# Kernel optimization log

Measured on AMD Instinct MI355X. Metric: run time of the kernel, lower is better.

## Reference

```python
import jax, jax.numpy as jnp
import numpy as np

EMBED_DIM = 1024
NUM_HEADS = 16
HEAD_DIM = EMBED_DIM // NUM_HEADS
N_PATCHES = 220
ROPE_BASE = 10000.0
EPS = 1e-6


def rms_norm(x, g):
    # x: [..., d]
    rms = jnp.sqrt(jnp.mean(x * x, axis=-1, keepdims=True) + EPS)
    return g * (x / rms)


def apply_rope(x):
    # torchtune-style interleaved RoPE. x: [b, s, h, d]
    b, s, h, d = x.shape
    theta = 1.0 / (ROPE_BASE ** (jnp.arange(0, d, 2, dtype=jnp.float32) / d))  # [d/2]
    ang = jnp.arange(s, dtype=jnp.float32)[:, None] * theta[None, :]           # [s, d/2]
    cos = jnp.cos(ang)[None, :, None, :]
    sin = jnp.sin(ang)[None, :, None, :]
    xs = x.reshape(b, s, h, d // 2, 2)
    x0, x1 = xs[..., 0], xs[..., 1]
    out = jnp.stack([x0 * cos - x1 * sin, x1 * cos + x0 * sin], axis=-1)
    return out.reshape(b, s, h, d).astype(x.dtype)


def attention_block(x, w_qkv, w_proj, b_proj, q_gain, k_gain):
    # x: [N, S, C]; one SDPA branch (shared by spatial & temporal paths)
    N, S, C = x.shape
    H, D = NUM_HEADS, HEAD_DIM
    qkv = jnp.einsum('nsc,ec->nse', x, w_qkv).reshape(N, S, 3, H, D)
    q, k, v = qkv[:, :, 0], qkv[:, :, 1], qkv[:, :, 2]  # [N, S, H, D]
    q = apply_rope(rms_norm(q, q_gain))
    k = apply_rope(rms_norm(k, k_gain))
    scale = 1.0 / jnp.sqrt(jnp.float32(D))
    scores = jnp.einsum('nqhd,nkhd->nhqk', q, k) * scale
    attn = jax.nn.softmax(scores, axis=-1)
    out = jnp.einsum('nhqk,nkhd->nqhd', attn, v).reshape(N, S, C)
    return jnp.einsum('nsc,ec->nse', out, w_proj) + b_proj


def setup_inputs() -> dict:
    key = jax.random.key(0)
    ks = jax.random.split(key, 8)
    E = EMBED_DIM
    sd = 1.0 / np.sqrt(E)
    x = jax.random.normal(ks[0], (4, 5280, E), dtype=jnp.float32)
    w_sqkv = jax.random.uniform(ks[1], (3 * E, E), jnp.float32, -sd, sd)
    w_sproj = jax.random.uniform(ks[2], (E, E), jnp.float32, -sd, sd)
    b_sproj = jax.random.uniform(ks[3], (E,), jnp.float32, -sd, sd)
    w_tqkv = jax.random.uniform(ks[4], (3 * E, E), jnp.float32, -sd, sd)
    w_tproj = jax.random.uniform(ks[5], (E, E), jnp.float32, -sd, sd)
    b_tproj = jax.random.uniform(ks[6], (E,), jnp.float32, -sd, sd)
    g = jnp.ones((HEAD_DIM,), jnp.float32)
    return {
        'x': x,
        'w_sqkv': w_sqkv, 'w_sproj': w_sproj, 'b_sproj': b_sproj,
        'w_tqkv': w_tqkv, 'w_tproj': w_tproj, 'b_tproj': b_tproj,
        'sq_gain': g, 'sk_gain': g, 'tq_gain': g, 'tk_gain': g,
    }


def reference(x, w_sqkv, w_sproj, b_sproj, w_tqkv, w_tproj, b_tproj,
              sq_gain, sk_gain, tq_gain, tk_gain):
    B, T, C = x.shape
    P = N_PATCHES
    F = T // P
    # spatial attention per frame: (b f) p c
    xs = x.reshape(B, F, P, C).reshape(B * F, P, C)
    out_s = attention_block(xs, w_sqkv, w_sproj, b_sproj, sq_gain, sk_gain)
    # temporal attention per patch: (b p) f c
    xt = out_s.reshape(B, F, P, C).transpose(0, 2, 1, 3).reshape(B * P, F, C)
    out_t = attention_block(xt, w_tqkv, w_tproj, b_tproj, tq_gain, tk_gain)
    # (b p) f c -> b (f p) c
    out = out_t.reshape(B, P, F, C).transpose(0, 2, 1, 3).reshape(B, F * P, C)
    return out
```

## Files before the change

kernel.cpp:

```cpp
#include <hip/hip_runtime.h>

typedef _Float16 f16;
typedef _Float16 f16x8 __attribute__((ext_vector_type(8)));
typedef f16x8 f16x8a __attribute__((may_alias));
typedef float f32x4 __attribute__((ext_vector_type(4)));

#define NTOK 21120
#define SCALE_Q 0.18033688f

__device__ __forceinline__ void gll16(const void* g, void* l) {
  __builtin_amdgcn_global_load_lds(
      (const __attribute__((address_space(1))) unsigned int*)g,
      (__attribute__((address_space(3))) unsigned int*)l, 16, 0, 0);
}

__device__ __forceinline__ unsigned int pack2(float a, float b) {
  union { f16 h[2]; unsigned int u; } c;
  c.h[0] = (f16)a; c.h[1] = (f16)b;
  return c.u;
}
__device__ __forceinline__ unsigned short f2h(float a) {
  union { f16 h; unsigned short u; } c; c.h = (f16)a; return c.u;
}

__global__ __launch_bounds__(256) void cast_kernel(
    const float* __restrict__ in, unsigned short* __restrict__ out, int n4) {
  int i = blockIdx.x * 256 + threadIdx.x;
  if (i >= n4) return;
  float4 v = ((const float4*)in)[i];
  uint2 o;
  o.x = pack2(v.x, v.y);
  o.y = pack2(v.z, v.w);
  ((uint2*)out)[i] = o;
}

__global__ __launch_bounds__(256) void transpose_cast_kernel(
    const float* __restrict__ in, unsigned short* __restrict__ out) {
  __shared__ float tile[32][33];
  int bx = blockIdx.x & 31, by = blockIdx.x >> 5;
  int tx = threadIdx.x & 31, ty = threadIdx.x >> 5;
#pragma unroll
  for (int i = 0; i < 32; i += 8)
    tile[ty + i][tx] = in[(size_t)(by * 32 + ty + i) * 1024 + bx * 32 + tx];
  __syncthreads();
#pragma unroll
  for (int i = 0; i < 32; i += 8)
    out[(size_t)(bx * 32 + ty + i) * 1024 + by * 32 + tx] = f2h(tile[tx][ty + i]);
}

__global__ __launch_bounds__(256) void bias_combine_kernel(
    const float* __restrict__ w, const float* __restrict__ b, float* __restrict__ bc) {
  int e = blockIdx.x * 256 + threadIdx.x;
  if (e >= 3072) return;
  const float4* wr = (const float4*)(w + (size_t)e * 1024);
  const float4* b4 = (const float4*)b;
  float s = 0.f;
  for (int c = 0; c < 256; ++c) {
    float4 wv = wr[c], bv = b4[c];
    s += wv.x * bv.x + wv.y * bv.y + wv.z * bv.z + wv.w * bv.w;
  }
  bc[e] = s;
}

__global__ __launch_bounds__(256) void rope_table_kernel(float2* tabS, float2* tabT) {
  int t = blockIdx.x * 256 + threadIdx.x;
  const float lb = logf(10000.0f) * (1.0f / 32.0f);
  if (t < 220 * 32) {
    int s = t >> 5, i = t & 31;
    float theta = expf(-(float)i * lb);
    float ang = (float)s * theta;
    tabS[t] = make_float2(cosf(ang), sinf(ang));
  } else if (t < 220 * 32 + 24 * 32) {
    int u = t - 220 * 32;
    int s = u >> 5, i = u & 31;
    float theta = expf(-(float)i * lb);
    float ang = (float)s * theta;
    tabT[u] = make_float2(cosf(ang), sinf(ang));
  }
}

__global__ __launch_bounds__(256) void gemm_bt(
    const unsigned short* __restrict__ A, const unsigned short* __restrict__ B,
    const float* __restrict__ bias, void* __restrict__ C,
    int M, int N, int K, int outmode,
    const float2* __restrict__ tab, const float* __restrict__ gq,
    const float* __restrict__ gk, int mode) {
  __shared__ __align__(16) unsigned short sh[16384];
  unsigned short* As = sh;
  unsigned short* Bs = sh + 8192;
  const int tid = threadIdx.x;
  const int w = tid >> 6, lane = tid & 63;
  const int l15 = lane & 15, quad = lane >> 4;
  const int wr = w >> 1, wc = w & 1;

  const int ntn = N >> 7;
  const int stride = ntn << 3;
  const int g = blockIdx.x / stride, r = blockIdx.x % stride;
  const int tn = r % ntn, tm = g * 8 + r / ntn;

  f32x4 acc[4][4];
#pragma unroll
  for (int a = 0; a < 4; ++a)
#pragma unroll
    for (int b = 0; b < 4; ++b) acc[a][b] = (f32x4){0.f, 0.f, 0.f, 0.f};

  const int srow = tid >> 3;
  const int schk = tid & 7;
  const size_t arow0 = (size_t)tm * 128;
  const size_t brow0 = (size_t)tn * 128;
  const int nk = K >> 6;

  for (int kt = 0; kt < nk; ++kt) {
    __syncthreads();
    const int kb = kt << 6;
#pragma unroll
    for (int rd = 0; rd < 4; ++rd) {
      int row = rd * 32 + srow;
      int sc = (schk ^ (row & 7)) * 8;
      gll16(A + (arow0 + row) * K + kb + sc, (char*)As + rd * 4096 + tid * 16);
      gll16(B + (brow0 + row) * K + kb + sc, (char*)Bs + rd * 4096 + tid * 16);
    }
    __syncthreads();
#pragma unroll
    for (int kk = 0; kk < 2; ++kk) {
      f16x8 af[4], bf[4];
#pragma unroll
      for (int mt = 0; mt < 4; ++mt) {
        int ra = wr * 64 + mt * 16 + l15;
        af[mt] = *(const f16x8a*)((const char*)As + ra * 128 + (((kk * 4 + quad) ^ (ra & 7)) * 16));
        int rb = wc * 64 + mt * 16 + l15;
        bf[mt] = *(const f16x8a*)((const char*)Bs + rb * 128 + (((kk * 4 + quad) ^ (rb & 7)) * 16));
      }
#pragma unroll
      for (int mt = 0; mt < 4; ++mt)
#pragma unroll
        for (int nt = 0; nt < 4; ++nt)
          acc[mt][nt] = __builtin_amdgcn_mfma_f32_16x16x32_f16(af[mt], bf[nt], acc[mt][nt], 0, 0, 0);
    }
  }

  float bv[4];
#pragma unroll
  for (int nt = 0; nt < 4; ++nt) bv[nt] = 0.f;
  if (bias != nullptr && outmode != 3) {
#pragma unroll
    for (int nt = 0; nt < 4; ++nt) bv[nt] = bias[tn * 128 + wc * 64 + nt * 16 + l15];
  }

  if (outmode == 2) {
    float* shf = (float*)sh;
#pragma unroll
    for (int mt = 0; mt < 4; ++mt) {
      __syncthreads();
#pragma unroll
      for (int nt = 0; nt < 4; ++nt)
#pragma unroll
        for (int rg = 0; rg < 4; ++rg)
          shf[(wr * 16 + quad * 4 + rg) * 132 + wc * 64 + nt * 16 + l15] = acc[mt][nt][rg] + bv[nt];
      __syncthreads();
      int l = tid >> 3, c8 = tid & 7;
      int grow = tm * 128 + ((l >> 4) << 6) + mt * 16 + (l & 15);
      float4* dst = (float4*)((float*)C + (size_t)grow * N + tn * 128 + c8 * 16);
      const float4* srcp = (const float4*)(shf + l * 132 + c8 * 16);
#pragma unroll
      for (int c = 0; c < 4; ++c) dst[c] = srcp[c];
    }
    return;
  }

  if (outmode == 3 && tn < 16) {
    const int qtile = tn < 8;
    const float* gg = qtile ? gq : gk;
    float* shf = (float*)sh;
    const int sub = tid & 3, pr = tid >> 2;
    const int l = pr >> 1, head = pr & 1;
    float bl[16];
    if (bias != nullptr) {
      const float4* bsrc = (const float4*)(bias + tn * 128 + head * 64 + sub * 16);
#pragma unroll
      for (int c = 0; c < 4; ++c) {
        float4 bb = bsrc[c];
        bl[c * 4 + 0] = bb.x; bl[c * 4 + 1] = bb.y; bl[c * 4 + 2] = bb.z; bl[c * 4 + 3] = bb.w;
      }
    } else {
#pragma unroll
      for (int j = 0; j < 16; ++j) bl[j] = 0.f;
    }
#pragma unroll
    for (int mt = 0; mt < 4; ++mt) {
      __syncthreads();
#pragma unroll
      for (int nt = 0; nt < 4; ++nt)
#pragma unroll
        for (int rg = 0; rg < 4; ++rg)
          shf[(wr * 16 + quad * 4 + rg) * 132 + wc * 64 + nt * 16 + l15] = acc[mt][nt][rg];
      __syncthreads();
      int grow = tm * 128 + ((l >> 4) << 6) + mt * 16 + (l & 15);
      int pos = (mode == 0) ? (grow % 220) : ((grow / 220) % 24);
      float v[16];
      const float4* vsrc = (const float4*)(shf + l * 132 + head * 64 + sub * 16);
#pragma unroll
      for (int c = 0; c < 4; ++c) {
        float4 t4 = vsrc[c];
        v[c * 4 + 0] = t4.x + bl[c * 4 + 0];
        v[c * 4 + 1] = t4.y + bl[c * 4 + 1];
        v[c * 4 + 2] = t4.z + bl[c * 4 + 2];
        v[c * 4 + 3] = t4.w + bl[c * 4 + 3];
      }
      float ssq = 0.f;
#pragma unroll
      for (int j = 0; j < 16; ++j) ssq += v[j] * v[j];
      ssq += __shfl_xor(ssq, 1);
      ssq += __shfl_xor(ssq, 2);
      float rr = rsqrtf(ssq * (1.0f / 64.0f) + 1e-6f);
      if (qtile) rr *= SCALE_Q;
      const float2* cs = tab + pos * 32 + sub * 8;
      const float2* g2 = (const float2*)gg + sub * 8;
      unsigned int o8[8];
#pragma unroll
      for (int jj = 0; jj < 8; ++jj) {
        float2 c = cs[jj], gp = g2[jj];
        float a = v[2 * jj] * rr * gp.x, b = v[2 * jj + 1] * rr * gp.y;
        o8[jj] = pack2(a * c.x - b * c.y, b * c.x + a * c.y);
      }
      unsigned short* dstp = (unsigned short*)C + (size_t)grow * N + tn * 128 + head * 64 + sub * 16;
      ((uint4*)dstp)[0] = ((const uint4*)o8)[0];
      ((uint4*)dstp)[1] = ((const uint4*)o8)[1];
    }
    return;
  }

  if (outmode == 3 && bias != nullptr) {
#pragma unroll
    for (int nt = 0; nt < 4; ++nt) bv[nt] = bias[tn * 128 + wc * 64 + nt * 16 + l15];
  }

  unsigned short* Cs = (unsigned short*)C;
#pragma unroll
  for (int p = 0; p < 2; ++p) {
    __syncthreads();
#pragma unroll
    for (int mi = 0; mi < 2; ++mi) {
      int mt = p * 2 + mi;
      int rl = wr * 32 + mi * 16 + quad * 4;
#pragma unroll
      for (int nt = 0; nt < 4; ++nt) {
        int cl = wc * 64 + nt * 16 + l15;
#pragma unroll
        for (int rg = 0; rg < 4; ++rg)
          sh[(rl + rg) * 136 + cl] = f2h(acc[mt][nt][rg] + bv[nt]);
      }
    }
    __syncthreads();
#pragma unroll
    for (int c = 0; c < 4; ++c) {
      int rl = c * 16 + (tid >> 4), cx = tid & 15;
      int grow = tm * 128 + ((rl >> 5) << 6) + p * 32 + (rl & 31);
      uint4 v = *(const uint4*)&sh[rl * 136 + cx * 8];
      *(uint4*)&Cs[(size_t)grow * N + tn * 128 + cx * 8] = v;
    }
  }
}

__global__ __launch_bounds__(256) void attn_spatial(
    const unsigned short* __restrict__ qkv, unsigned short* __restrict__ aout) {
  __shared__ __align__(16) unsigned short sh[30720];
  unsigned short* Kls = sh;
  unsigned short* Vt = sh + 8192;
  unsigned short* P = sh + 22528;
  const int tid = threadIdx.x;
  const int w = tid >> 6, lane = tid & 63;
  const int l15 = lane & 15, quad = lane >> 4;
  const int n = blockIdx.x >> 4, h = blockIdx.x & 15;
  const size_t tb = (size_t)n * 220;
  const unsigned short* qbase = qkv + tb * 3072 + h * 64;

  f16x8 aq[4][2];
#pragma unroll
  for (int mt = 0; mt < 4; ++mt) {
    int row = w * 64 + mt * 16 + l15;
    if (row > 219) row = 219;
#pragma unroll
    for (int c = 0; c < 2; ++c)
      aq[mt][c] = *(const f16x8a*)(qbase + (size_t)row * 3072 + c * 32 + quad * 8);
  }
  if (tid < 220) {
    const uint4* src = (const uint4*)(qbase + (size_t)tid * 3072 + 2048);
    uint4 vv[8];
#pragma unroll
    for (int c = 0; c < 8; ++c) vv[c] = src[c];
    const unsigned short* us = (const unsigned short*)vv;
#pragma unroll
    for (int d = 0; d < 64; ++d) Vt[d * 224 + tid] = us[d];
  } else if (tid < 224) {
#pragma unroll
    for (int d = 0; d < 64; ++d) Vt[d * 224 + tid] = 0;
  }

  float lsum[4][4];
  f32x4 o[4][4];
#pragma unroll
  for (int mt = 0; mt < 4; ++mt)
#pragma unroll
    for (int rg = 0; rg < 4; ++rg) lsum[mt][rg] = 0.f;
#pragma unroll
  for (int mt = 0; mt < 4; ++mt)
#pragma unroll
    for (int nt = 0; nt < 4; ++nt) o[mt][nt] = (f32x4){0.f, 0.f, 0.f, 0.f};

  const int xr = (l15 & 3) ^ ((l15 >> 2) & 3);
  unsigned short* Pw = P + w * 2048;

  for (int half = 0; half < 2; ++half) {
    const int k0 = half * 128;
    const int nslot = half ? 736 : 1024;
#pragma unroll
    for (int k = 0; k < 4; ++k) {
      int slot = k * 256 + tid;
      if (slot < nslot) {
        int rl = slot >> 3, c = slot & 7;
        gll16(qbase + (size_t)(k0 + rl) * 3072 + 1024 + ((c ^ (rl & 7)) * 8),
              (char*)Kls + k * 4096 + w * 1024);
      }
    }
    __syncthreads();
    const int nci = half ? 3 : 4;
    for (int ci = 0; ci < nci; ++ci) {
      const int cig = half * 4 + ci;
      f16x8 bk[2][2];
#pragma unroll
      for (int ct = 0; ct < 2; ++ct) {
        int rl = ci * 32 + ct * 16 + l15;
#pragma unroll
        for (int c = 0; c < 2; ++c)
          bk[ct][c] = *(const f16x8a*)((const char*)Kls + rl * 128 + (((quad + 4 * c) ^ (rl & 7)) * 16));
      }
      f32x4 sc[4][2];
#pragma unroll
      for (int mt = 0; mt < 4; ++mt)
#pragma unroll
        for (int ct = 0; ct < 2; ++ct) {
          f32x4 z = (f32x4){0.f, 0.f, 0.f, 0.f};
          z = __builtin_amdgcn_mfma_f32_16x16x32_f16(aq[mt][0], bk[ct][0], z, 0, 0, 0);
          sc[mt][ct] = __builtin_amdgcn_mfma_f32_16x16x32_f16(aq[mt][1], bk[ct][1], z, 0, 0, 0);
        }
      const int okk = (cig * 32 + 16 + l15) < 220;
#pragma unroll
      for (int mt = 0; mt < 4; ++mt)
#pragma unroll
        for (int rg = 0; rg < 4; ++rg) {
          float p0 = exp2f(sc[mt][0][rg]);
          float p1 = okk ? exp2f(sc[mt][1][rg]) : 0.0f;
          lsum[mt][rg] += p0 + p1;
          int xw = quad ^ rg;
          unsigned short* pb = Pw + (mt * 16 + quad * 4 + rg) * 32;
          pb[(((l15 >> 3) ^ xw) * 8) + (l15 & 7)] = f2h(p0);
          pb[(((2 + (l15 >> 3)) ^ xw) * 8) + (l15 & 7)] = f2h(p1);
        }
      __asm__ volatile("s_waitcnt lgkmcnt(0)" ::: "memory");
      f16x8 ap[4], bv[4];
#pragma unroll
      for (int mt = 0; mt < 4; ++mt)
        ap[mt] = *(const f16x8a*)((const char*)Pw + (mt * 16 + l15) * 64 + (quad ^ xr) * 16);
#pragma unroll
      for (int nt = 0; nt < 4; ++nt)
        bv[nt] = *(const f16x8a*)((const char*)Vt + (nt * 16 + l15) * 448 + cig * 64 + quad * 16);
#pragma unroll
      for (int mt = 0; mt < 4; ++mt)
#pragma unroll
        for (int nt = 0; nt < 4; ++nt)
          o[mt][nt] = __builtin_amdgcn_mfma_f32_16x16x32_f16(ap[mt], bv[nt], o[mt][nt], 0, 0, 0);
    }
    __syncthreads();
  }

#pragma unroll
  for (int mt = 0; mt < 4; ++mt)
#pragma unroll
    for (int rg = 0; rg < 4; ++rg) {
      float l = lsum[mt][rg];
      l += __shfl_xor(l, 1);
      l += __shfl_xor(l, 2);
      l += __shfl_xor(l, 4);
      l += __shfl_xor(l, 8);
      int s = w * 64 + mt * 16 + quad * 4 + rg;
      if (s < 220) {
        float inv = 1.0f / l;
        unsigned short* dst = aout + (tb + s) * 1024 + h * 64;
#pragma unroll
        for (int nt = 0; nt < 4; ++nt) dst[nt * 16 + l15] = f2h(o[mt][nt][rg] * inv);
      }
    }
}

__global__ __launch_bounds__(256) void attn_temporal(
    const unsigned short* __restrict__ qkv, unsigned short* __restrict__ aout) {
  __shared__ __align__(16) unsigned short sh[14336];
  const int tid = threadIdx.x;
  const int w = tid >> 6, lane = tid & 63;
  const int l15 = lane & 15, quad = lane >> 4;
  const int b = blockIdx.x / 880;
  const int rem = blockIdx.x % 880;
  const int p = rem >> 2, hq = rem & 3;
  const int h = hq * 4 + w;
  unsigned short* Vtw = sh + w * 2560;
  unsigned short* Pw = sh + 10240 + w * 1024;
  const unsigned short* base = qkv + ((size_t)(b * 24) * 220 + p) * 3072 + h * 64;
  const size_t fs = (size_t)220 * 3072;

  {
    int r = lane >> 1, hf = lane & 1;
    if (r < 24) {
      const uint4* src = (const uint4*)(base + r * fs + 2048 + hf * 32);
      uint4 vv[4];
#pragma unroll
      for (int c = 0; c < 4; ++c) vv[c] = src[c];
      const unsigned short* us = (const unsigned short*)vv;
#pragma unroll
      for (int j = 0; j < 32; ++j) Vtw[(hf * 32 + j) * 40 + r] = us[j];
    } else {
#pragma unroll
      for (int j = 0; j < 32; ++j) Vtw[(hf * 32 + j) * 40 + r] = 0;
    }
  }
  f16x8 aq[2][2], bk[2][2];
#pragma unroll
  for (int mt = 0; mt < 2; ++mt) {
    int row = mt * 16 + l15;
    if (row > 23) row = 23;
#pragma unroll
    for (int c = 0; c < 2; ++c)
      aq[mt][c] = *(const f16x8a*)(base + row * fs + c * 32 + quad * 8);
  }
#pragma unroll
  for (int ct = 0; ct < 2; ++ct) {
    int row = ct * 16 + l15;
    if (row > 23) row = 23;
#pragma unroll
    for (int c = 0; c < 2; ++c)
      bk[ct][c] = *(const f16x8a*)(base + row * fs + 1024 + c * 32 + quad * 8);
  }
  f32x4 sc[2][2];
#pragma unroll
  for (int mt = 0; mt < 2; ++mt)
#pragma unroll
    for (int ct = 0; ct < 2; ++ct) {
      f32x4 z = (f32x4){0.f, 0.f, 0.f, 0.f};
      z = __builtin_amdgcn_mfma_f32_16x16x32_f16(aq[mt][0], bk[ct][0], z, 0, 0, 0);
      sc[mt][ct] = __builtin_amdgcn_mfma_f32_16x16x32_f16(aq[mt][1], bk[ct][1], z, 0, 0, 0);
    }
  const int xr = (l15 & 3) ^ ((l15 >> 2) & 3);
  const int okk = l15 < 8;
  float lr[2][4];
#pragma unroll
  for (int mt = 0; mt < 2; ++mt)
#pragma unroll
    for (int rg = 0; rg < 4; ++rg) {
      float p0 = exp2f(sc[mt][0][rg]);
      float p1 = okk ? exp2f(sc[mt][1][rg]) : 0.0f;
      float rs = p0 + p1;
      rs += __shfl_xor(rs, 1);
      rs += __shfl_xor(rs, 2);
      rs += __shfl_xor(rs, 4);
      rs += __shfl_xor(rs, 8);
      lr[mt][rg] = rs;
      int xw = quad ^ rg;
      unsigned short* pb = Pw + (mt * 16 + quad * 4 + rg) * 32;
      pb[(((l15 >> 3) ^ xw) * 8) + (l15 & 7)] = f2h(p0);
      pb[(((2 + (l15 >> 3)) ^ xw) * 8) + (l15 & 7)] = f2h(p1);
    }
  __asm__ volatile("s_waitcnt lgkmcnt(0)" ::: "memory");
  f16x8 ap[2], bv[4];
#pragma unroll
  for (int mt = 0; mt < 2; ++mt)
    ap[mt] = *(const f16x8a*)((const char*)Pw + (mt * 16 + l15) * 64 + (quad ^ xr) * 16);
#pragma unroll
  for (int nt = 0; nt < 4; ++nt)
    bv[nt] = *(const f16x8a*)((const char*)Vtw + (nt * 16 + l15) * 80 + quad * 16);
  f32x4 o[2][4];
#pragma unroll
  for (int mt = 0; mt < 2; ++mt)
#pragma unroll
    for (int nt = 0; nt < 4; ++nt) {
      f32x4 z = (f32x4){0.f, 0.f, 0.f, 0.f};
      o[mt][nt] = __builtin_amdgcn_mfma_f32_16x16x32_f16(ap[mt], bv[nt], z, 0, 0, 0);
    }
#pragma unroll
  for (int mt = 0; mt < 2; ++mt)
#pragma unroll
    for (int rg = 0; rg < 4; ++rg) {
      int s = mt * 16 + quad * 4 + rg;
      if (s < 24) {
        float inv = 1.0f / lr[mt][rg];
        unsigned short* dst = aout + ((size_t)(b * 24 + s) * 220 + p) * 1024 + h * 64;
#pragma unroll
        for (int nt = 0; nt < 4; ++nt) dst[nt * 16 + l15] = f2h(o[mt][nt][rg] * inv);
      }
    }
}

extern "C" void kernel_launch(void* const* d_in, const int* in_sizes, int n_in,
                              void* d_out, int out_size, void* d_ws, size_t ws_size,
                              hipStream_t stream) {
  (void)in_sizes; (void)n_in; (void)out_size; (void)ws_size;
  const float* x = (const float*)d_in[0];
  const float* wsqkv = (const float*)d_in[1];
  const float* wsproj = (const float*)d_in[2];
  const float* bsproj = (const float*)d_in[3];
  const float* wtqkv = (const float*)d_in[4];
  const float* wtproj = (const float*)d_in[5];
  const float* btproj = (const float*)d_in[6];
  const float* sqg = (const float*)d_in[7];
  const float* skg = (const float*)d_in[8];
  const float* tqg = (const float*)d_in[9];
  const float* tkg = (const float*)d_in[10];

  char* ws = (char*)d_ws;
  size_t off = 0;
  auto alloc = [&](size_t bytes) {
    char* ptr = ws + off;
    off += (bytes + 255) & ~(size_t)255;
    return ptr;
  };
  unsigned short* xb = (unsigned short*)alloc((size_t)NTOK * 1024 * 2);
  unsigned short* qkvb = (unsigned short*)alloc((size_t)NTOK * 3072 * 2);
  unsigned short* aoutb = (unsigned short*)alloc((size_t)NTOK * 1024 * 2);
  unsigned short* wsqkvb = (unsigned short*)alloc((size_t)3072 * 1024 * 2);
  unsigned short* wsprojTb = (unsigned short*)alloc((size_t)1024 * 1024 * 2);
  unsigned short* wtqkvb = (unsigned short*)alloc((size_t)3072 * 1024 * 2);
  unsigned short* wtprojb = (unsigned short*)alloc((size_t)1024 * 1024 * 2);
  unsigned short* wcb = (unsigned short*)alloc((size_t)3072 * 1024 * 2);
  float* bcb = (float*)alloc(3072 * 4);
  float2* tabS = (float2*)alloc(220 * 32 * 8);
  float2* tabT = (float2*)alloc(24 * 32 * 8);

  dim3 blk(256);
  cast_kernel<<<21120, blk, 0, stream>>>(x, xb, 5406720);
  cast_kernel<<<3072, blk, 0, stream>>>(wsqkv, wsqkvb, 786432);
  cast_kernel<<<3072, blk, 0, stream>>>(wtqkv, wtqkvb, 786432);
  cast_kernel<<<1024, blk, 0, stream>>>(wtproj, wtprojb, 262144);
  transpose_cast_kernel<<<1024, blk, 0, stream>>>(wsproj, wsprojTb);
  bias_combine_kernel<<<12, blk, 0, stream>>>(wtqkv, bsproj, bcb);
  rope_table_kernel<<<31, blk, 0, stream>>>(tabS, tabT);

  gemm_bt<<<dim3(24 * 8), blk, 0, stream>>>(wtqkvb, wsprojTb, nullptr, wcb, 3072, 1024, 1024, 0,
                                            nullptr, nullptr, nullptr, 0);

  gemm_bt<<<dim3(165 * 24), blk, 0, stream>>>(xb, wsqkvb, nullptr, qkvb, NTOK, 3072, 1024, 3,
                                              tabS, sqg, skg, 0);
  attn_spatial<<<dim3(1536), blk, 0, stream>>>(qkvb, aoutb);
  gemm_bt<<<dim3(165 * 24), blk, 0, stream>>>(aoutb, wcb, bcb, qkvb, NTOK, 3072, 1024, 3,
                                              tabT, tqg, tkg, 1);
  attn_temporal<<<dim3(3520), blk, 0, stream>>>(qkvb, aoutb);
  gemm_bt<<<dim3(165 * 8), blk, 0, stream>>>(aoutb, wtprojb, btproj, (float*)d_out, NTOK, 1024, 1024, 2,
                                             nullptr, nullptr, nullptr, 0);
}
```

Measured before the change: 811.3 us.

## Replace 128-tile GEMMs with 256x256 pipelined 512-thread GEMM kernel

Adds a new GEMM kernel with 256x256 tiles, 8 waves, a four-slot LDS ring fed by global_load_lds and explicit vmcnt waits, s_setprio around MFMA bursts, and XCD-aware workgroup remapping. The fused RMSNorm+RoPE and fp32 epilogues are moved into the new kernel, using DPP cross-lane reductions. The activation buffers are padded to a multiple of 256 rows and the pad is zeroed so the last tile can read past the real rows without bounds checks. The goal is more data reuse per tile and better overlap of loads with MFMA. The cost is 128 KB of LDS per block, higher register pressure, and extra memset launches.

```diff
diff --git a/kernel.cpp b/kernel.cpp
--- a/kernel.cpp
+++ b/kernel.cpp
@@ -6,6 +6,7 @@
 typedef float f32x4 __attribute__((ext_vector_type(4)));
 
 #define NTOK 21120
+#define MPAD 21248
 #define SCALE_Q 0.18033688f
 
 __device__ __forceinline__ void gll16(const void* g, void* l) {
@@ -21,6 +22,14 @@
 }
 __device__ __forceinline__ unsigned short f2h(float a) {
   union { f16 h; unsigned short u; } c; c.h = (f16)a; return c.u;
+}
+
+template <int C>
+__device__ __forceinline__ float dppf(float x) {
+  union { float f; int i; } u, r;
+  u.f = x;
+  r.i = __builtin_amdgcn_update_dpp(0, u.i, C, 0xf, 0xf, true);
+  return r.f;
 }
 
 __global__ __launch_bounds__(256) void cast_kernel(
@@ -139,102 +148,6 @@
     }
   }
 
-  float bv[4];
-#pragma unroll
-  for (int nt = 0; nt < 4; ++nt) bv[nt] = 0.f;
-  if (bias != nullptr && outmode != 3) {
-#pragma unroll
-    for (int nt = 0; nt < 4; ++nt) bv[nt] = bias[tn * 128 + wc * 64 + nt * 16 + l15];
-  }
-
-  if (outmode == 2) {
-    float* shf = (float*)sh;
-#pragma unroll
-    for (int mt = 0; mt < 4; ++mt) {
-      __syncthreads();
-#pragma unroll
-      for (int nt = 0; nt < 4; ++nt)
-#pragma unroll
-        for (int rg = 0; rg < 4; ++rg)
-          shf[(wr * 16 + quad * 4 + rg) * 132 + wc * 64 + nt * 16 + l15] = acc[mt][nt][rg] + bv[nt];
-      __syncthreads();
-      int l = tid >> 3, c8 = tid & 7;
-      int grow = tm * 128 + ((l >> 4) << 6) + mt * 16 + (l & 15);
-      float4* dst = (float4*)((float*)C + (size_t)grow * N + tn * 128 + c8 * 16);
-      const float4* srcp = (const float4*)(shf + l * 132 + c8 * 16);
-#pragma unroll
-      for (int c = 0; c < 4; ++c) dst[c] = srcp[c];
-    }
-    return;
-  }
-
-  if (outmode == 3 && tn < 16) {
-    const int qtile = tn < 8;
-    const float* gg = qtile ? gq : gk;
-    float* shf = (float*)sh;
-    const int sub = tid & 3, pr = tid >> 2;
-    const int l = pr >> 1, head = pr & 1;
-    float bl[16];
-    if (bias != nullptr) {
-      const float4* bsrc = (const float4*)(bias + tn * 128 + head * 64 + sub * 16);
-#pragma unroll
-      for (int c = 0; c < 4; ++c) {
-        float4 bb = bsrc[c];
-        bl[c * 4 + 0] = bb.x; bl[c * 4 + 1] = bb.y; bl[c * 4 + 2] = bb.z; bl[c * 4 + 3] = bb.w;
-      }
-    } else {
-#pragma unroll
-      for (int j = 0; j < 16; ++j) bl[j] = 0.f;
-    }
-#pragma unroll
-    for (int mt = 0; mt < 4; ++mt) {
-      __syncthreads();
-#pragma unroll
-      for (int nt = 0; nt < 4; ++nt)
-#pragma unroll
-        for (int rg = 0; rg < 4; ++rg)
-          shf[(wr * 16 + quad * 4 + rg) * 132 + wc * 64 + nt * 16 + l15] = acc[mt][nt][rg];
-      __syncthreads();
-      int grow = tm * 128 + ((l >> 4) << 6) + mt * 16 + (l & 15);
-      int pos = (mode == 0) ? (grow % 220) : ((grow / 220) % 24);
-      float v[16];
-      const float4* vsrc = (const float4*)(shf + l * 132 + head * 64 + sub * 16);
-#pragma unroll
-      for (int c = 0; c < 4; ++c) {
-        float4 t4 = vsrc[c];
-        v[c * 4 + 0] = t4.x + bl[c * 4 + 0];
-        v[c * 4 + 1] = t4.y + bl[c * 4 + 1];
-        v[c * 4 + 2] = t4.z + bl[c * 4 + 2];
-        v[c * 4 + 3] = t4.w + bl[c * 4 + 3];
-      }
-      float ssq = 0.f;
-#pragma unroll
-      for (int j = 0; j < 16; ++j) ssq += v[j] * v[j];
-      ssq += __shfl_xor(ssq, 1);
-      ssq += __shfl_xor(ssq, 2);
-      float rr = rsqrtf(ssq * (1.0f / 64.0f) + 1e-6f);
-      if (qtile) rr *= SCALE_Q;
-      const float2* cs = tab + pos * 32 + sub * 8;
-      const float2* g2 = (const float2*)gg + sub * 8;
-      unsigned int o8[8];
-#pragma unroll
-      for (int jj = 0; jj < 8; ++jj) {
-        float2 c = cs[jj], gp = g2[jj];
-        float a = v[2 * jj] * rr * gp.x, b = v[2 * jj + 1] * rr * gp.y;
-        o8[jj] = pack2(a * c.x - b * c.y, b * c.x + a * c.y);
-      }
-      unsigned short* dstp = (unsigned short*)C + (size_t)grow * N + tn * 128 + head * 64 + sub * 16;
-      ((uint4*)dstp)[0] = ((const uint4*)o8)[0];
-      ((uint4*)dstp)[1] = ((const uint4*)o8)[1];
-    }
-    return;
-  }
-
-  if (outmode == 3 && bias != nullptr) {
-#pragma unroll
-    for (int nt = 0; nt < 4; ++nt) bv[nt] = bias[tn * 128 + wc * 64 + nt * 16 + l15];
-  }
-
   unsigned short* Cs = (unsigned short*)C;
 #pragma unroll
   for (int p = 0; p < 2; ++p) {
@@ -248,7 +161,7 @@
         int cl = wc * 64 + nt * 16 + l15;
 #pragma unroll
         for (int rg = 0; rg < 4; ++rg)
-          sh[(rl + rg) * 136 + cl] = f2h(acc[mt][nt][rg] + bv[nt]);
+          sh[(rl + rg) * 136 + cl] = f2h(acc[mt][nt][rg]);
       }
     }
     __syncthreads();
@@ -258,6 +171,257 @@
       int grow = tm * 128 + ((rl >> 5) << 6) + p * 32 + (rl & 31);
       uint4 v = *(const uint4*)&sh[rl * 136 + cx * 8];
       *(uint4*)&Cs[(size_t)grow * N + tn * 128 + cx * 8] = v;
+    }
+  }
+}
+
+#define FENCE() asm volatile("" ::: "memory")
+#define BAR() do { FENCE(); __builtin_amdgcn_s_barrier(); FENCE(); } while (0)
+#define WAITV(N) asm volatile("s_waitcnt vmcnt(" #N ")" ::: "memory")
+#define LDA(sl, i) (*(const f16x8a*)(As + (sl) * 16384 + sA[i]))
+#define LDB(sl, i) (*(const f16x8a*)(Bs + (sl) * 16384 + sB[i]))
+#define STAGE_A(u, sl) do { \
+    gll16(aS0 + (size_t)(u) * 32, As + (sl) * 16384 + tid * 16); \
+    gll16(aS1 + (size_t)(u) * 32, As + (sl) * 16384 + 8192 + tid * 16); \
+  } while (0)
+#define STAGE_B(u, sl) do { \
+    gll16(bS0 + (size_t)(u) * 32, Bs + (sl) * 16384 + tid * 16); \
+    gll16(bS1 + (size_t)(u) * 32, Bs + (sl) * 16384 + 8192 + tid * 16); \
+  } while (0)
+#define MM16(QB, A0_, A1_, A2_, A3_, B0_, B1_, B2_, B3_) do { \
+    acc[QB + 0][0] = __builtin_amdgcn_mfma_f32_16x16x32_f16(A0_, B0_, acc[QB + 0][0], 0, 0, 0); \
+    acc[QB + 0][1] = __builtin_amdgcn_mfma_f32_16x16x32_f16(A0_, B1_, acc[QB + 0][1], 0, 0, 0); \
+    acc[QB + 0][2] = __builtin_amdgcn_mfma_f32_16x16x32_f16(A0_, B2_, acc[QB + 0][2], 0, 0, 0); \
+    acc[QB + 0][3] = __builtin_amdgcn_mfma_f32_16x16x32_f16(A0_, B3_, acc[QB + 0][3], 0, 0, 0); \
+    acc[QB + 1][0] = __builtin_amdgcn_mfma_f32_16x16x32_f16(A1_, B0_, acc[QB + 1][0], 0, 0, 0); \
+    acc[QB + 1][1] = __builtin_amdgcn_mfma_f32_16x16x32_f16(A1_, B1_, acc[QB + 1][1], 0, 0, 0); \
+    acc[QB + 1][2] = __builtin_amdgcn_mfma_f32_16x16x32_f16(A1_, B2_, acc[QB + 1][2], 0, 0, 0); \
+    acc[QB + 1][3] = __builtin_amdgcn_mfma_f32_16x16x32_f16(A1_, B3_, acc[QB + 1][3], 0, 0, 0); \
+    acc[QB + 2][0] = __builtin_amdgcn_mfma_f32_16x16x32_f16(A2_, B0_, acc[QB + 2][0], 0, 0, 0); \
+    acc[QB + 2][1] = __builtin_amdgcn_mfma_f32_16x16x32_f16(A2_, B1_, acc[QB + 2][1], 0, 0, 0); \
+    acc[QB + 2][2] = __builtin_amdgcn_mfma_f32_16x16x32_f16(A2_, B2_, acc[QB + 2][2], 0, 0, 0); \
+    acc[QB + 2][3] = __builtin_amdgcn_mfma_f32_16x16x32_f16(A2_, B3_, acc[QB + 2][3], 0, 0, 0); \
+    acc[QB + 3][0] = __builtin_amdgcn_mfma_f32_16x16x32_f16(A3_, B0_, acc[QB + 3][0], 0, 0, 0); \
+    acc[QB + 3][1] = __builtin_amdgcn_mfma_f32_16x16x32_f16(A3_, B1_, acc[QB + 3][1], 0, 0, 0); \
+    acc[QB + 3][2] = __builtin_amdgcn_mfma_f32_16x16x32_f16(A3_, B2_, acc[QB + 3][2], 0, 0, 0); \
+    acc[QB + 3][3] = __builtin_amdgcn_mfma_f32_16x16x32_f16(A3_, B3_, acc[QB + 3][3], 0, 0, 0); \
+  } while (0)
+
+__global__ __launch_bounds__(512, 2) void gemm256(
+    const unsigned short* __restrict__ A, const unsigned short* __restrict__ B,
+    const float* __restrict__ bias, void* __restrict__ C,
+    int M, int N, int K, int outmode,
+    const float2* __restrict__ tab, const float* __restrict__ gq,
+    const float* __restrict__ gk, int mode) {
+  extern __shared__ char smem[];
+  char* As = smem;
+  char* Bs = smem + 65536;
+  const int tid = threadIdx.x;
+  const int w = tid >> 6, lane = tid & 63;
+  const int l15 = lane & 15, quad = lane >> 4;
+  const int wr = w >> 2, wc = w & 3;
+
+  const int nwg = gridDim.x;
+  const int qd = nwg >> 3, rm = nwg & 7;
+  const int xcd = blockIdx.x & 7, lin = blockIdx.x >> 3;
+  const int wgid = (xcd < rm ? xcd * (qd + 1) : rm * (qd + 1) + (xcd - rm) * qd) + lin;
+  const int ntn = N >> 8;
+  const int stg = ntn << 3;
+  const int g = wgid / stg, r2 = wgid % stg;
+  const int tn = r2 % ntn, tm = g * 8 + r2 / ntn;
+
+  int sA[8], sB[4];
+#pragma unroll
+  for (int mt = 0; mt < 8; ++mt) {
+    int ra = wr * 128 + mt * 16 + l15;
+    sA[mt] = ra * 64 + ((quad ^ ((ra >> 1) & 3)) << 4);
+  }
+#pragma unroll
+  for (int nt = 0; nt < 4; ++nt) {
+    int rb = wc * 64 + nt * 16 + l15;
+    sB[nt] = rb * 64 + ((quad ^ ((rb >> 1) & 3)) << 4);
+  }
+
+  const int srow = tid >> 2;
+  const int ssw = ((tid & 3) ^ ((tid >> 3) & 3)) << 3;
+  const unsigned short* aS0 = A + (size_t)(tm * 256 + srow) * K + ssw;
+  const unsigned short* aS1 = A + (size_t)(tm * 256 + 128 + srow) * K + ssw;
+  const unsigned short* bS0 = B + (size_t)(tn * 256 + srow) * K + ssw;
+  const unsigned short* bS1 = B + (size_t)(tn * 256 + 128 + srow) * K + ssw;
+
+  f32x4 acc[8][4];
+#pragma unroll
+  for (int i = 0; i < 8; ++i)
+#pragma unroll
+    for (int j = 0; j < 4; ++j) acc[i][j] = (f32x4){0.f, 0.f, 0.f, 0.f};
+
+  STAGE_A(0, 0); STAGE_B(0, 0);
+  STAGE_A(1, 1); STAGE_B(1, 1);
+  STAGE_A(2, 2); STAGE_B(2, 2);
+  WAITV(8);
+  BAR();
+
+#pragma unroll 2
+  for (int t = 0; t < 16; ++t) {
+    const int s0 = (t & 1) << 1, s1 = s0 | 1, st3 = s0 ^ 3;
+    const int u3 = 2 * t + 3;
+    f16x8 b0, b1, b2, b3;
+    b0 = LDB(s0, 0); b1 = LDB(s0, 1); b2 = LDB(s0, 2); b3 = LDB(s0, 3);
+    {
+      f16x8 a0 = LDA(s0, 0), a1 = LDA(s0, 1), a2 = LDA(s0, 2), a3 = LDA(s0, 3);
+      if (t <= 14) STAGE_A(u3, st3);
+      BAR();
+      __builtin_amdgcn_s_setprio(1);
+      MM16(0, a0, a1, a2, a3, b0, b1, b2, b3);
+      __builtin_amdgcn_s_setprio(0);
+      BAR();
+    }
+    {
+      f16x8 a0 = LDA(s0, 4), a1 = LDA(s0, 5), a2 = LDA(s0, 6), a3 = LDA(s0, 7);
+      if (t <= 14) STAGE_B(u3, st3);
+      BAR();
+      __builtin_amdgcn_s_setprio(1);
+      MM16(4, a0, a1, a2, a3, b0, b1, b2, b3);
+      __builtin_amdgcn_s_setprio(0);
+      if (t <= 14) { WAITV(8); } else { WAITV(0); }
+      BAR();
+    }
+    b0 = LDB(s1, 0); b1 = LDB(s1, 1); b2 = LDB(s1, 2); b3 = LDB(s1, 3);
+    {
+      f16x8 a0 = LDA(s1, 0), a1 = LDA(s1, 1), a2 = LDA(s1, 2), a3 = LDA(s1, 3);
+      if (t <= 13) STAGE_A(u3 + 1, s0);
+      BAR();
+      __builtin_amdgcn_s_setprio(1);
+      MM16(0, a0, a1, a2, a3, b0, b1, b2, b3);
+      __builtin_amdgcn_s_setprio(0);
+      BAR();
+    }
+    {
+      f16x8 a0 = LDA(s1, 4), a1 = LDA(s1, 5), a2 = LDA(s1, 6), a3 = LDA(s1, 7);
+      if (t <= 13) STAGE_B(u3 + 1, s0);
+      BAR();
+      __builtin_amdgcn_s_setprio(1);
+      MM16(4, a0, a1, a2, a3, b0, b1, b2, b3);
+      __builtin_amdgcn_s_setprio(0);
+      if (t <= 13) { WAITV(8); } else if (t == 14) { WAITV(4); }
+      BAR();
+    }
+  }
+
+  BAR();
+  const size_t grow0 = (size_t)tm * 256 + wr * 128;
+  const int gcol0 = tn * 256 + wc * 64;
+
+  float bl[4] = {0.f, 0.f, 0.f, 0.f};
+  if (bias != nullptr) {
+#pragma unroll
+    for (int nt = 0; nt < 4; ++nt) bl[nt] = bias[gcol0 + nt * 16 + l15];
+  }
+
+  if (outmode == 2) {
+    float* wf = (float*)(smem + w * 16384);
+    const int frow = lane >> 4, fc = lane & 15;
+#pragma unroll
+    for (int h = 0; h < 2; ++h) {
+#pragma unroll
+      for (int mi = 0; mi < 4; ++mi)
+#pragma unroll
+        for (int nt = 0; nt < 4; ++nt)
+#pragma unroll
+          for (int rg = 0; rg < 4; ++rg) {
+            int row = mi * 16 + quad * 4 + rg;
+            int col = nt * 16 + l15;
+            int c = col >> 2, lo = col & 3;
+            wf[row * 64 + ((c ^ (row & 15)) << 2) + lo] = acc[h * 4 + mi][nt][rg] + bl[nt];
+          }
+#pragma unroll
+      for (int it = 0; it < 16; ++it) {
+        int row = it * 4 + frow;
+        float4 v = *(const float4*)(wf + row * 64 + ((fc ^ (row & 15)) << 2));
+        size_t gr = grow0 + h * 64 + row;
+        if (gr < (size_t)M)
+          *(float4*)((float*)C + gr * N + gcol0 + fc * 4) = v;
+      }
+    }
+    return;
+  }
+
+  unsigned short* wh = (unsigned short*)(smem + w * 16384);
+  if (outmode == 3 && tn < 8) {
+    const int isQ = tn < 4;
+    const float* gg = isQ ? gq : gk;
+    float gv[4];
+#pragma unroll
+    for (int nt = 0; nt < 4; ++nt) gv[nt] = gg[nt * 16 + l15];
+#pragma unroll
+    for (int mt = 0; mt < 8; ++mt) {
+      float v[4][4], rr[4];
+#pragma unroll
+      for (int rg = 0; rg < 4; ++rg) rr[rg] = 0.f;
+#pragma unroll
+      for (int nt = 0; nt < 4; ++nt)
+#pragma unroll
+        for (int rg = 0; rg < 4; ++rg) {
+          float x = acc[mt][nt][rg] + bl[nt];
+          v[nt][rg] = x;
+          rr[rg] += x * x;
+        }
+#pragma unroll
+      for (int rg = 0; rg < 4; ++rg) {
+        float s = rr[rg];
+        s += dppf<0xB1>(s);
+        s += dppf<0x4E>(s);
+        s += dppf<0x141>(s);
+        s += dppf<0x140>(s);
+        float r = rsqrtf(s * (1.0f / 64.0f) + 1e-6f);
+        rr[rg] = isQ ? r * SCALE_Q : r;
+      }
+      int pos[4];
+#pragma unroll
+      for (int rg = 0; rg < 4; ++rg) {
+        int grow = (int)grow0 + mt * 16 + quad * 4 + rg;
+        pos[rg] = mode ? ((grow / 220) % 24) : (grow % 220);
+      }
+#pragma unroll
+      for (int nt = 0; nt < 4; ++nt) {
+        int col = nt * 16 + l15;
+        int ii = nt * 8 + (l15 >> 1);
+        int c = col >> 3, lo = col & 7;
+#pragma unroll
+        for (int rg = 0; rg < 4; ++rg) {
+          float2 cs = tab[pos[rg] * 32 + ii];
+          float x = v[nt][rg] * rr[rg] * gv[nt];
+          float p = dppf<0xB1>(x);
+          float o = (l15 & 1) ? (x * cs.x + p * cs.y) : (x * cs.x - p * cs.y);
+          int row = mt * 16 + quad * 4 + rg;
+          wh[row * 64 + ((c ^ (row & 7)) << 3) + lo] = f2h(o);
+        }
+      }
+    }
+  } else {
+#pragma unroll
+    for (int mt = 0; mt < 8; ++mt)
+#pragma unroll
+      for (int nt = 0; nt < 4; ++nt) {
+        int col = nt * 16 + l15;
+        int c = col >> 3, lo = col & 7;
+#pragma unroll
+        for (int rg = 0; rg < 4; ++rg) {
+          int row = mt * 16 + quad * 4 + rg;
+          wh[row * 64 + ((c ^ (row & 7)) << 3) + lo] = f2h(acc[mt][nt][rg] + bl[nt]);
+        }
+      }
+  }
+  {
+    const int frow = lane >> 3, fch = lane & 7;
+    unsigned short* C16 = (unsigned short*)C;
+#pragma unroll
+    for (int it = 0; it < 16; ++it) {
+      int row = it * 8 + frow;
+      uint4 vv = *(const uint4*)((const char*)wh + row * 128 + ((fch ^ (row & 7)) << 4));
+      size_t gr = grow0 + row;
+      if (gr < (size_t)M)
+        *(uint4*)(C16 + gr * N + gcol0 + fch * 8) = vv;
     }
   }
 }
@@ -515,6 +679,13 @@
   const float* tqg = (const float*)d_in[9];
   const float* tkg = (const float*)d_in[10];
 
+  static bool attr_done = false;
+  if (!attr_done) {
+    hipFuncSetAttribute(reinterpret_cast<const void*>(gemm256),
+                        hipFuncAttributeMaxDynamicSharedMemorySize, 131072);
+    attr_done = true;
+  }
+
   char* ws = (char*)d_ws;
   size_t off = 0;
   auto alloc = [&](size_t bytes) {
@@ -522,9 +693,9 @@
     off += (bytes + 255) & ~(size_t)255;
     return ptr;
   };
-  unsigned short* xb = (unsigned short*)alloc((size_t)NTOK * 1024 * 2);
+  unsigned short* xb = (unsigned short*)alloc((size_t)MPAD * 1024 * 2);
   unsigned short* qkvb = (unsigned short*)alloc((size_t)NTOK * 3072 * 2);
-  unsigned short* aoutb = (unsigned short*)alloc((size_t)NTOK * 1024 * 2);
+  unsigned short* aoutb = (unsigned short*)alloc((size_t)MPAD * 1024 * 2);
   unsigned short* wsqkvb = (unsigned short*)alloc((size_t)3072 * 1024 * 2);
   unsigned short* wsprojTb = (unsigned short*)alloc((size_t)1024 * 1024 * 2);
   unsigned short* wtqkvb = (unsigned short*)alloc((size_t)3072 * 1024 * 2);
@@ -534,6 +705,9 @@
   float2* tabS = (float2*)alloc(220 * 32 * 8);
   float2* tabT = (float2*)alloc(24 * 32 * 8);
 
+  hipMemsetAsync(xb + (size_t)NTOK * 1024, 0, (size_t)(MPAD - NTOK) * 1024 * 2, stream);
+  hipMemsetAsync(aoutb + (size_t)NTOK * 1024, 0, (size_t)(MPAD - NTOK) * 1024 * 2, stream);
+
   dim3 blk(256);
   cast_kernel<<<21120, blk, 0, stream>>>(x, xb, 5406720);
   cast_kernel<<<3072, blk, 0, stream>>>(wsqkv, wsqkvb, 786432);
@@ -546,12 +720,14 @@
   gemm_bt<<<dim3(24 * 8), blk, 0, stream>>>(wtqkvb, wsprojTb, nullptr, wcb, 3072, 1024, 1024, 0,
                                             nullptr, nullptr, nullptr, 0);
 
-  gemm_bt<<<dim3(165 * 24), blk, 0, stream>>>(xb, wsqkvb, nullptr, qkvb, NTOK, 3072, 1024, 3,
-                                              tabS, sqg, skg, 0);
+  dim3 blk512(512);
+  gemm256<<<dim3(83 * 12), blk512, 131072, stream>>>(xb, wsqkvb, nullptr, qkvb, NTOK, 3072, 1024, 3,
+                                                     tabS, sqg, skg, 0);
   attn_spatial<<<dim3(1536), blk, 0, stream>>>(qkvb, aoutb);
-  gemm_bt<<<dim3(165 * 24), blk, 0, stream>>>(aoutb, wcb, bcb, qkvb, NTOK, 3072, 1024, 3,
-                                              tabT, tqg, tkg, 1);
+  gemm256<<<dim3(83 * 12), blk512, 131072, stream>>>(aoutb, wcb, bcb, qkvb, NTOK, 3072, 1024, 3,
+                                                     tabT, tqg, tkg, 1);
   attn_temporal<<<dim3(3520), blk, 0, stream>>>(qkvb, aoutb);
-  gemm_bt<<<dim3(165 * 8), blk, 0, stream>>>(aoutb, wtprojb, btproj, (float*)d_out, NTOK, 1024, 1024, 2,
-                                             nullptr, nullptr, nullptr, 0);
-}
+  gemm256<<<dim3(83 * 4), blk512, 131072, stream>>>(aoutb, wtprojb, btproj, (float*)d_out,
+                                                    NTOK, 1024, 1024, 2,
+                                                    nullptr, nullptr, nullptr, 0);
+}
```

New measurement: 760.0 us. 1.07x faster.
